# Kernel optimization log

Measured on AMD Instinct MI355X. Metric: run time of the kernel, lower is better.

## Reference

```python
import jax, jax.numpy as jnp
import numpy as np
from jax import lax

HIDDEN = 256      # hidden_dim
LATENT = 128      # latent_dim
VOCAB = 32000     # vocab_size
MAX_LEN = 64      # max_len (stack capacity guard, as in original)
MAX_STEPS = 128   # fixed step budget for the decode stack machine
N_NODES = 511     # complete binary tree, depth 9


def _linear_params(key, fan_in, fan_out):
    k1, k2 = jax.random.split(key)
    s = 1.0 / np.sqrt(fan_in)
    W = jax.random.uniform(k1, (fan_out, fan_in), minval=-s, maxval=s, dtype=jnp.float32)
    b = jax.random.uniform(k2, (fan_out,), minval=-s, maxval=s, dtype=jnp.float32)
    return W, b


def setup_inputs() -> dict:
    key = jax.random.key(0)
    ks = jax.random.split(key, 10)
    embed = jax.random.normal(ks[0], (VOCAB, HIDDEN), dtype=jnp.float32)
    Wpar, bpar = _linear_params(ks[1], 3 * HIDDEN, HIDDEN)
    Wmu, bmu = _linear_params(ks[2], HIDDEN, LATENT)
    Wlv, blv = _linear_params(ks[3], HIDDEN, LATENT)
    W1, b1 = _linear_params(ks[4], LATENT, HIDDEN)
    W2, b2 = _linear_params(ks[5], HIDDEN, HIDDEN + 1)
    Wl, bl = _linear_params(ks[6], HIDDEN, VOCAB)
    Wp, bp = _linear_params(ks[7], HIDDEN, 2 * LATENT + VOCAB)
    values = jax.random.randint(ks[8], (N_NODES,), 0, VOCAB)
    idx = np.arange(N_NODES)
    left = np.where(2 * idx + 1 < N_NODES, 2 * idx + 1, -1).astype(np.int32)
    right = np.where(2 * idx + 2 < N_NODES, 2 * idx + 2, -1).astype(np.int32)
    eps = jax.random.normal(ks[9], (LATENT,), dtype=jnp.float32)
    return dict(embed=embed, Wpar=Wpar, bpar=bpar, Wmu=Wmu, bmu=bmu,
                Wlv=Wlv, blv=blv, W1=W1, b1=b1, W2=W2, b2=b2,
                Wl=Wl, bl=bl, Wp=Wp, bp=bp, eps=eps,
                values=jnp.asarray(values), left=jnp.asarray(left), right=jnp.asarray(right))


def reference(embed, Wpar, bpar, Wmu, bmu, Wlv, blv, W1, b1, W2, b2,
              Wl, bl, Wp, bp, eps, values, left, right):
    # ---------- encode: bottom-up over tree stored as index arrays ----------
    emb = embed[values]  # [N, H], one gather for all node embeddings

    def enc_step(h, i):
        v = emb[i]
        li = jnp.maximum(left[i], 0)
        ri = jnp.maximum(right[i], 0)
        cat = jnp.concatenate([v, h[li], h[ri]])          # [3H]
        hp = cat @ Wpar.T + bpar                           # parent combine
        hi = jnp.where(left[i] < 0, v, hp)                 # leaf -> embedding
        return h.at[i].set(hi), None

    h0 = jnp.zeros((values.shape[0], HIDDEN), dtype=embed.dtype)
    # children have larger index than parents -> process in descending order
    h, _ = lax.scan(enc_step, h0, jnp.arange(values.shape[0] - 1, -1, -1))
    root = h[0]
    mu = root @ Wmu.T + bmu
    logvar = root @ Wlv.T + blv
    z = mu + eps * jnp.exp(0.5 * logvar)                   # reparameterize

    # ---------- decode: stack machine with fixed step budget ----------
    V, L = VOCAB, LATENT
    stack0 = jnp.zeros((MAX_LEN, L), dtype=z.dtype).at[0].set(z)
    out0 = jnp.zeros((MAX_STEPS, V), dtype=z.dtype)

    def dec_step(state, _):
        stack, sp, out, op = state
        active = sp > 0
        idx = jnp.maximum(sp - 1, 0)
        node = stack[idx]                                  # pop
        hmid = jax.nn.leaky_relu(node @ W1.T + b1, 0.2)
        co = hmid @ W2.T + b2                              # [H+1]; co[0] = gate
        is_parent = (co[0] > 0) & (sp - 1 <= MAX_LEN - 2) & active

        def parent_fn(_):
            dec = co[1:] @ Wp.T + bp                       # [V + 2L]
            value = dec[:V]
            ll = dec[V:V + L]
            rl = dec[V + L:]
            # original appends llatent then rlatent -> rlatent on top
            st = stack.at[idx].set(ll).at[idx + 1].set(rl)
            return value, st, sp + 1

        def leaf_fn(_):
            return co[1:] @ Wl.T + bl, stack, sp - 1

        value, st, nsp = lax.cond(is_parent, parent_fn, leaf_fn, None)
        m = active.astype(z.dtype)
        out = out.at[op].add(m * value)                    # rows written once
        stack = jnp.where(active, st, stack)
        sp = jnp.where(active, nsp, sp)
        op = op + active.astype(op.dtype)
        return (stack, sp, out, op), None

    init = (stack0, jnp.int32(1), out0, jnp.int32(0))
    (_, _, out, _), _ = lax.scan(dec_step, init, None, length=MAX_STEPS)
    return out, mu, logvar
```

## Files before the change

kernel.cpp:

```cpp
#include <hip/hip_runtime.h>

#define HID 256
#define LAT 128
#define VOC 32000
#define NSTEP 128

__global__ __launch_bounds__(512)
void prep_kernel(const float* __restrict__ Wp, const float* __restrict__ W2,
                 const float* __restrict__ b2, const float* __restrict__ bp,
                 const float* __restrict__ Wpar,
                 const float* __restrict__ Wmu, const float* __restrict__ Wlv,
                 float* __restrict__ Wcomb, float* __restrict__ bcomb,
                 float* __restrict__ Wq_par, float* __restrict__ Wq_mu,
                 float* __restrict__ Wq_lv, float* __restrict__ Wq_w2) {
    const int b = blockIdx.x;
    const int t = threadIdx.x;
    if (b < 256) {
        const int o = b;
        const int k = t & 255, jh = t >> 8;
        __shared__ float wpt_s[256];
        __shared__ float part_s[2][256];
        __shared__ float red_s[4];
        if (t < 256) wpt_s[t] = Wp[(size_t)(VOC + o) * HID + t];
        __syncthreads();
        float acc = 0.f;
#pragma unroll 8
        for (int j = 0; j < 128; j++)
            acc += wpt_s[jh * 128 + j] * W2[(size_t)(1 + jh * 128 + j) * HID + k];
        part_s[jh][k] = acc;
        if (t < 256) {
            float p = wpt_s[k] * b2[1 + k];
            p += __shfl_xor(p, 1);  p += __shfl_xor(p, 2);  p += __shfl_xor(p, 4);
            p += __shfl_xor(p, 8);  p += __shfl_xor(p, 16); p += __shfl_xor(p, 32);
            if ((k & 63) == 0) red_s[k >> 6] = p;
        }
        __syncthreads();
        if (t < 256) Wcomb[(size_t)o * HID + k] = part_s[0][k] + part_s[1][k];
        if (t == 0) bcomb[o] = bp[VOC + o] + red_s[0] + red_s[1] + red_s[2] + red_s[3];
    } else if (b < 352) {
        const int k4 = (b - 256) * 2 + (t >> 8);
        const int r = t & 255;
        ((float4*)Wq_par)[k4 * 256 + r] = *(const float4*)(Wpar + (size_t)r * 768 + 4 * k4);
    } else if (b < 384) {
        const int k4 = (b - 352) * 2 + (t >> 8);
        const int r = t & 127, sel = (t >> 7) & 1;
        const float* src = (sel ? Wlv : Wmu) + (size_t)r * HID + 4 * k4;
        ((float4*)(sel ? Wq_lv : Wq_mu))[k4 * 128 + r] = *(const float4*)src;
    } else {
        const int k4 = (b - 384) * 2 + (t >> 8);
        const int r = t & 255;
        ((float4*)Wq_w2)[k4 * 256 + r] = *(const float4*)(W2 + (size_t)(1 + r) * HID + 4 * k4);
    }
}

__global__ __launch_bounds__(1024)
void enc2(const float* __restrict__ embed, const int* __restrict__ values,
          const float* __restrict__ Wq, const float* __restrict__ bpar,
          float* __restrict__ h, int base) {
    const int i = base + blockIdx.x;
    const int t = threadIdx.x;
    const int o = t & 255;
    const int g = t >> 8;
    const int cid = g & 1, kh = g >> 1;
    __shared__ __align__(16) float cat[2][768];
    __shared__ float part[4][256];
    __shared__ __align__(16) float pcat[768];

    const int c0n = 2 * i + 1;
    for (int q = t; q < 1536; q += 1024) {
        const int cc = (q >= 768);
        const int e = q - cc * 768;
        const int node = c0n + cc;
        const int seg = e >> 8, idx = e & 255;
        float v;
        if (seg == 0) v = embed[(size_t)values[node] * HID + idx];
        else {
            const int ch = 2 * node + seg;
            v = (ch >= 255) ? embed[(size_t)values[ch] * HID + idx]
                            : h[(size_t)ch * HID + idx];
        }
        cat[cc][e] = v;
    }
    __syncthreads();
    {
        const float4* wq = (const float4*)Wq + o;
        const float4* c4 = (const float4*)cat[cid] + kh * 96;
        float s0 = 0.f, s1 = 0.f, s2 = 0.f, s3 = 0.f;
#pragma unroll 8
        for (int k4 = 0; k4 < 96; k4 += 4) {
            const float4 wa = wq[(size_t)(kh * 96 + k4) * 256];
            const float4 wb = wq[(size_t)(kh * 96 + k4 + 1) * 256];
            const float4 wc = wq[(size_t)(kh * 96 + k4 + 2) * 256];
            const float4 wd = wq[(size_t)(kh * 96 + k4 + 3) * 256];
            const float4 ca = c4[k4], cb = c4[k4 + 1], cx = c4[k4 + 2], cd = c4[k4 + 3];
            s0 = fmaf(wa.x, ca.x, s0); s0 = fmaf(wa.y, ca.y, s0);
            s0 = fmaf(wa.z, ca.z, s0); s0 = fmaf(wa.w, ca.w, s0);
            s1 = fmaf(wb.x, cb.x, s1); s1 = fmaf(wb.y, cb.y, s1);
            s1 = fmaf(wb.z, cb.z, s1); s1 = fmaf(wb.w, cb.w, s1);
            s2 = fmaf(wc.x, cx.x, s2); s2 = fmaf(wc.y, cx.y, s2);
            s2 = fmaf(wc.z, cx.z, s2); s2 = fmaf(wc.w, cx.w, s2);
            s3 = fmaf(wd.x, cd.x, s3); s3 = fmaf(wd.y, cd.y, s3);
            s3 = fmaf(wd.z, cd.z, s3); s3 = fmaf(wd.w, cd.w, s3);
        }
        part[g][o] = (s0 + s1) + (s2 + s3);
    }
    __syncthreads();
    if (t < 512) {
        const int c = t >> 8;
        pcat[256 + (c << 8) + o] = part[c][o] + part[c + 2][o] + bpar[o];
    } else if (t < 768) {
        const int idx = t & 255;
        pcat[idx] = embed[(size_t)values[i] * HID + idx];
    }
    __syncthreads();
    {
        const float4* wq = (const float4*)Wq + o;
        const float4* c4 = (const float4*)pcat + g * 48;
        float s0 = 0.f, s1 = 0.f, s2 = 0.f, s3 = 0.f;
#pragma unroll
        for (int k4 = 0; k4 < 48; k4 += 4) {
            const float4 wa = wq[(size_t)(g * 48 + k4) * 256];
            const float4 wb = wq[(size_t)(g * 48 + k4 + 1) * 256];
            const float4 wc = wq[(size_t)(g * 48 + k4 + 2) * 256];
            const float4 wd = wq[(size_t)(g * 48 + k4 + 3) * 256];
            const float4 ca = c4[k4], cb = c4[k4 + 1], cx = c4[k4 + 2], cd = c4[k4 + 3];
            s0 = fmaf(wa.x, ca.x, s0); s0 = fmaf(wa.y, ca.y, s0);
            s0 = fmaf(wa.z, ca.z, s0); s0 = fmaf(wa.w, ca.w, s0);
            s1 = fmaf(wb.x, cb.x, s1); s1 = fmaf(wb.y, cb.y, s1);
            s1 = fmaf(wb.z, cb.z, s1); s1 = fmaf(wb.w, cb.w, s1);
            s2 = fmaf(wc.x, cx.x, s2); s2 = fmaf(wc.y, cx.y, s2);
            s2 = fmaf(wc.z, cx.z, s2); s2 = fmaf(wc.w, cx.w, s2);
            s3 = fmaf(wd.x, cd.x, s3); s3 = fmaf(wd.y, cd.y, s3);
            s3 = fmaf(wd.z, cd.z, s3); s3 = fmaf(wd.w, cd.w, s3);
        }
        part[g][o] = (s0 + s1) + (s2 + s3);
    }
    __syncthreads();
    if (t < 256)
        h[(size_t)i * HID + t] = part[0][t] + part[1][t] + part[2][t] + part[3][t] + bpar[t];
}

__global__ __launch_bounds__(256)
void enc_lvl(const float* __restrict__ embed, const int* __restrict__ values,
             const float* __restrict__ Wq, const float* __restrict__ bpar,
             float* __restrict__ h, int first, int logS) {
    const int S = 1 << logS;
    const int R = 256 >> logS;
    const int node = first + (blockIdx.x >> logS);
    const int slice = blockIdx.x & (S - 1);
    const int t = threadIdx.x;
    const int rl = t & (R - 1);
    const int g = t >> (8 - logS);
    __shared__ __align__(16) float cat_s[768];
    __shared__ float part_s[256];

    for (int e = t; e < 768; e += 256) {
        const int seg = e >> 8, idx = e & 255;
        cat_s[e] = (seg == 0) ? embed[(size_t)values[node] * HID + idx]
                              : h[(size_t)(2 * node + seg) * HID + idx];
    }
    __syncthreads();

    const int r0 = slice * R;
    const int nk4 = 192 >> logS;
    const float4* wq = (const float4*)Wq + (size_t)(g * nk4) * 256 + r0 + rl;
    const float4* c4 = (const float4*)cat_s + g * nk4;
    float s0 = 0.f, s1 = 0.f, s2 = 0.f, s3 = 0.f;
    for (int k4 = 0; k4 < nk4; k4 += 4) {
        const float4 wa = wq[(size_t)(k4) * 256];
        const float4 wb = wq[(size_t)(k4 + 1) * 256];
        const float4 wc = wq[(size_t)(k4 + 2) * 256];
        const float4 wd = wq[(size_t)(k4 + 3) * 256];
        const float4 ca = c4[k4], cb = c4[k4 + 1], cx = c4[k4 + 2], cd = c4[k4 + 3];
        s0 = fmaf(wa.x, ca.x, s0); s0 = fmaf(wa.y, ca.y, s0);
        s0 = fmaf(wa.z, ca.z, s0); s0 = fmaf(wa.w, ca.w, s0);
        s1 = fmaf(wb.x, cb.x, s1); s1 = fmaf(wb.y, cb.y, s1);
        s1 = fmaf(wb.z, cb.z, s1); s1 = fmaf(wb.w, cb.w, s1);
        s2 = fmaf(wc.x, cx.x, s2); s2 = fmaf(wc.y, cx.y, s2);
        s2 = fmaf(wc.z, cx.z, s2); s2 = fmaf(wc.w, cx.w, s2);
        s3 = fmaf(wd.x, cd.x, s3); s3 = fmaf(wd.y, cd.y, s3);
        s3 = fmaf(wd.z, cd.z, s3); s3 = fmaf(wd.w, cd.w, s3);
    }
    part_s[t] = (s0 + s1) + (s2 + s3);
    __syncthreads();
    if (t < R) {
        float v = bpar[r0 + t];
        for (int g2 = 0; g2 < S; g2++) v += part_s[g2 * R + t];
        h[(size_t)node * HID + r0 + t] = v;
    }
}

__global__ __launch_bounds__(512, 2)
void recur_kernel(const float* W1, const float* b1,
                  const float* W2, const float* b2,
                  const float* Wcomb, const float* bcomb,
                  const float* embed, const int* values,
                  const float* Wq_par, const float* bpar,
                  const float* h,
                  const float* Wq_mu, const float* bmu,
                  const float* Wq_lv, const float* blv,
                  const float* eps, float* out,
                  float* Hrec, int* rowflag) {
    const int t = threadIdx.x;
    const int o = t >> 1;
    const int hk = t & 1;
    __shared__ __align__(16) float stack_s[64 * 128];
    __shared__ __align__(16) float hmid_s[256];
    __shared__ __align__(16) float cat0_s[768];
    __shared__ float c0part_s[8];

    float4 w1r[16];
#pragma unroll
    for (int j = 0; j < 16; j++)
        w1r[j] = *(const float4*)(W1 + (size_t)o * 128 + hk * 64 + 4 * j);
    float4 wcr[32];
#pragma unroll
    for (int j = 0; j < 32; j++)
        wcr[j] = *(const float4*)(Wcomb + (size_t)o * 256 + hk * 128 + 4 * j);

    const float b1o = b1[o];
    const float bco = bcomb[o];
    const float b20 = b2[0];
    const float w2o = W2[o];

    const int v0 = values[0];
    for (int e = t; e < 768; e += 512) {
        const int seg = e >> 8, idx = e & 255;
        cat0_s[e] = (seg == 0) ? embed[(size_t)v0 * HID + idx]
                               : h[(size_t)seg * HID + idx];
    }
    __syncthreads();
    {
        const float4* wq = (const float4*)Wq_par + (size_t)(hk * 96) * 256 + o;
        const float4* c4 = (const float4*)cat0_s + hk * 96;
        float s0 = 0.f, s1 = 0.f, s2 = 0.f, s3 = 0.f;
        for (int k4 = 0; k4 < 96; k4 += 4) {
            const float4 wa = wq[(size_t)(k4) * 256];
            const float4 wb = wq[(size_t)(k4 + 1) * 256];
            const float4 wc = wq[(size_t)(k4 + 2) * 256];
            const float4 wd = wq[(size_t)(k4 + 3) * 256];
            const float4 ca = c4[k4], cb = c4[k4 + 1], cx = c4[k4 + 2], cd = c4[k4 + 3];
            s0 = fmaf(wa.x, ca.x, s0); s0 = fmaf(wa.y, ca.y, s0);
            s0 = fmaf(wa.z, ca.z, s0); s0 = fmaf(wa.w, ca.w, s0);
            s1 = fmaf(wb.x, cb.x, s1); s1 = fmaf(wb.y, cb.y, s1);
            s1 = fmaf(wb.z, cb.z, s1); s1 = fmaf(wb.w, cb.w, s1);
            s2 = fmaf(wc.x, cx.x, s2); s2 = fmaf(wc.y, cx.y, s2);
            s2 = fmaf(wc.z, cx.z, s2); s2 = fmaf(wc.w, cx.w, s2);
            s3 = fmaf(wd.x, cd.x, s3); s3 = fmaf(wd.y, cd.y, s3);
            s3 = fmaf(wd.z, cd.z, s3); s3 = fmaf(wd.w, cd.w, s3);
        }
        float a = (s0 + s1) + (s2 + s3);
        a += __shfl_xor(a, 1);
        if (hk == 0) hmid_s[o] = a + bpar[o];
    }
    __syncthreads();

    {
        const int r = o & 127;
        const float4* wqh = (const float4*)(o < 128 ? Wq_mu : Wq_lv) + r;
        const float4* r4 = (const float4*)hmid_s + hk * 32;
        float s0 = 0.f, s1 = 0.f;
#pragma unroll
        for (int k4 = 0; k4 < 32; k4 += 2) {
            const float4 wa = wqh[(size_t)(hk * 32 + k4) * 128];
            const float4 wb = wqh[(size_t)(hk * 32 + k4 + 1) * 128];
            const float4 ca = r4[k4], cb = r4[k4 + 1];
            s0 = fmaf(wa.x, ca.x, s0); s0 = fmaf(wa.y, ca.y, s0);
            s0 = fmaf(wa.z, ca.z, s0); s0 = fmaf(wa.w, ca.w, s0);
            s1 = fmaf(wb.x, cb.x, s1); s1 = fmaf(wb.y, cb.y, s1);
            s1 = fmaf(wb.z, cb.z, s1); s1 = fmaf(wb.w, cb.w, s1);
        }
        float a = s0 + s1;
        a += __shfl_xor(a, 1);
        if (hk == 0) {
            const float v = a + (o < 128 ? bmu[o & 127] : blv[o & 127]);
            out[(size_t)NSTEP * VOC + o] = v;
            stack_s[128 + o] = v;
        }
    }
    __syncthreads();
    if (t < 128)
        stack_s[t] = stack_s[128 + t] + eps[t] * expf(0.5f * stack_s[256 + t]);

    int sp = 1, op = 0;
    unsigned long long pm0 = 0ULL, pm1 = 0ULL;
    __syncthreads();

    for (int step = 0; step < NSTEP; step++) {
        if (sp <= 0) break;
        const int idx = sp - 1;

        const float* np = stack_s + idx * 128 + hk * 64;
        float a0 = 0.f, a1 = 0.f;
#pragma unroll
        for (int j = 0; j < 16; j += 2) {
            const float4 v0r = *(const float4*)(np + 4 * j);
            const float4 v1r = *(const float4*)(np + 4 * j + 4);
            a0 = fmaf(w1r[j].x, v0r.x, a0);     a0 = fmaf(w1r[j].y, v0r.y, a0);
            a0 = fmaf(w1r[j].z, v0r.z, a0);     a0 = fmaf(w1r[j].w, v0r.w, a0);
            a1 = fmaf(w1r[j + 1].x, v1r.x, a1); a1 = fmaf(w1r[j + 1].y, v1r.y, a1);
            a1 = fmaf(w1r[j + 1].z, v1r.z, a1); a1 = fmaf(w1r[j + 1].w, v1r.w, a1);
        }
        float a = a0 + a1;
        a += __shfl_xor(a, 1);

        float act = a + b1o;
        act = act > 0.f ? act : 0.2f * act;
        float m = w2o * act;
        m += __shfl_xor(m, 2);  m += __shfl_xor(m, 4);  m += __shfl_xor(m, 8);
        m += __shfl_xor(m, 16); m += __shfl_xor(m, 32);
        if ((t & 63) == 0) c0part_s[t >> 6] = m;
        if (hk == 0) {
            hmid_s[o] = act;
            Hrec[(size_t)op * HID + o] = act;
        }
        __syncthreads();

        const float4 q0 = ((const float4*)c0part_s)[0];
        const float4 q1 = ((const float4*)c0part_s)[1];
        const float c = ((q0.x + q0.y) + (q0.z + q0.w)) +
                        ((q1.x + q1.y) + (q1.z + q1.w)) + b20;
        const bool par = (c > 0.f) && (sp <= 63);

        if (par) {
            const float* hp = hmid_s + hk * 128;
            float s0 = 0.f, s1 = 0.f, s2 = 0.f, s3 = 0.f;
#pragma unroll
            for (int j = 0; j < 32; j += 4) {
                const float4 v0r = *(const float4*)(hp + 4 * j);
                const float4 v1r = *(const float4*)(hp + 4 * j + 4);
                const float4 v2r = *(const float4*)(hp + 4 * j + 8);
                const float4 v3r = *(const float4*)(hp + 4 * j + 12);
                s0 = fmaf(wcr[j].x, v0r.x, s0);     s0 = fmaf(wcr[j].y, v0r.y, s0);
                s0 = fmaf(wcr[j].z, v0r.z, s0);     s0 = fmaf(wcr[j].w, v0r.w, s0);
                s1 = fmaf(wcr[j + 1].x, v1r.x, s1); s1 = fmaf(wcr[j + 1].y, v1r.y, s1);
                s1 = fmaf(wcr[j + 1].z, v1r.z, s1); s1 = fmaf(wcr[j + 1].w, v1r.w, s1);
                s2 = fmaf(wcr[j + 2].x, v2r.x, s2); s2 = fmaf(wcr[j + 2].y, v2r.y, s2);
                s2 = fmaf(wcr[j + 2].z, v2r.z, s2); s2 = fmaf(wcr[j + 2].w, v2r.w, s2);
                s3 = fmaf(wcr[j + 3].x, v3r.x, s3); s3 = fmaf(wcr[j + 3].y, v3r.y, s3);
                s3 = fmaf(wcr[j + 3].w, v3r.w, s3); s3 = fmaf(wcr[j + 3].z, v3r.z, s3);
            }
            float s = (s0 + s1) + (s2 + s3);
            s += __shfl_xor(s, 1);
            if (hk == 0)
                stack_s[(idx + (o >> 7)) * 128 + (o & 127)] = s + bco;
            if (op < 64) pm0 |= (1ULL << op); else pm1 |= (1ULL << (op - 64));
            sp += 1;
        } else {
            sp -= 1;
        }
        op++;
        __syncthreads();
    }

    if (t < 128) {
        int f = -1;
        if (t < op) f = (t < 64) ? (int)((pm0 >> t) & 1) : (int)((pm1 >> (t - 64)) & 1);
        rowflag[t] = f;
    }
}

__global__ __launch_bounds__(256)
void co1_kernel(const float* __restrict__ Hrec, const float* __restrict__ Wq_w2,
                const float* __restrict__ b2, const int* __restrict__ rowflag,
                float* __restrict__ Co1, int* __restrict__ lists) {
    const int r = blockIdx.x;
    const int c = threadIdx.x;
    if (r == 128) {
        if (c == 0) {
            int nl = 0, np_ = 0, nz = 0;
            for (int q = 0; q < 128; q++) {
                const int f = rowflag[q];
                if (f == 0) lists[nl++] = q;
                else if (f == 1) lists[128 + np_++] = q;
                else lists[256 + nz++] = q;
            }
            lists[384] = nl; lists[385] = np_; lists[386] = nz;
        }
        return;
    }
    __shared__ __align__(16) float hs[256];
    hs[c] = Hrec[(size_t)r * HID + c];
    __syncthreads();
    const float4* wq = (const float4*)Wq_w2 + c;
    const float4* h4 = (const float4*)hs;
    float s0 = b2[1 + c], s1 = 0.f, s2 = 0.f, s3 = 0.f;
#pragma unroll 8
    for (int k4 = 0; k4 < 64; k4 += 4) {
        const float4 a0 = wq[(k4) * 256],     h0 = h4[k4];
        const float4 a1 = wq[(k4 + 1) * 256], h1 = h4[k4 + 1];
        const float4 a2 = wq[(k4 + 2) * 256], h2 = h4[k4 + 2];
        const float4 a3 = wq[(k4 + 3) * 256], h3 = h4[k4 + 3];
        s0 = fmaf(a0.x, h0.x, s0); s0 = fmaf(a0.y, h0.y, s0);
        s0 = fmaf(a0.z, h0.z, s0); s0 = fmaf(a0.w, h0.w, s0);
        s1 = fmaf(a1.x, h1.x, s1); s1 = fmaf(a1.y, h1.y, s1);
        s1 = fmaf(a1.z, h1.z, s1); s1 = fmaf(a1.w, h1.w, s1);
        s2 = fmaf(a2.x, h2.x, s2); s2 = fmaf(a2.y, h2.y, s2);
        s2 = fmaf(a2.z, h2.z, s2); s2 = fmaf(a2.w, h2.w, s2);
        s3 = fmaf(a3.x, h3.x, s3); s3 = fmaf(a3.y, h3.y, s3);
        s3 = fmaf(a3.z, h3.z, s3); s3 = fmaf(a3.w, h3.w, s3);
    }
    Co1[(size_t)r * HID + c] = (s0 + s1) + (s2 + s3);
}

__global__ __launch_bounds__(256, 2)
void value_kernel(const float* __restrict__ Co1, const int* __restrict__ lists,
                  const float* __restrict__ Wl, const float* __restrict__ bl,
                  const float* __restrict__ Wp, const float* __restrict__ bp,
                  float* __restrict__ out) {
    const int m = blockIdx.y;
    const int t = threadIdx.x;
    const int v = blockIdx.x * 128 + (t & 127);
    const int rh = t >> 7;
    const int n = lists[384 + m];
    const int* list = lists + m * 128;
    const float* Wx = m ? Wp : Wl;
    const float* bx = m ? bp : bl;
    const float bv = bx[v];
    const float4* w4 = (const float4*)(Wx + (size_t)v * HID);

    for (int rc = 0; rc < n; rc += 32) {
        const int nr = min(32, n - rc);
        float acc[16];
#pragma unroll
        for (int i = 0; i < 16; i++) acc[i] = 0.f;
        for (int kc = 0; kc < 4; kc++) {
            float4 w[16];
#pragma unroll
            for (int i = 0; i < 16; i++) w[i] = w4[kc * 16 + i];
#pragma unroll
            for (int aa = 0; aa < 16; aa++) {
                const int rr = 2 * aa + rh;
                if (rr < nr) {
                    const int row = __builtin_amdgcn_readfirstlane(list[rc + rr]);
                    const float* cp = Co1 + (size_t)row * HID + kc * 64;
                    float s0 = 0.f, s1 = 0.f, s2 = 0.f, s3 = 0.f;
#pragma unroll
                    for (int i = 0; i < 16; i += 4) {
                        const float4 c0 = *(const float4*)(cp + 4 * i);
                        const float4 c1 = *(const float4*)(cp + 4 * i + 4);
                        const float4 c2 = *(const float4*)(cp + 4 * i + 8);
                        const float4 c3 = *(const float4*)(cp + 4 * i + 12);
                        s0 = fmaf(w[i].x, c0.x, s0);     s0 = fmaf(w[i].y, c0.y, s0);
                        s0 = fmaf(w[i].z, c0.z, s0);     s0 = fmaf(w[i].w, c0.w, s0);
                        s1 = fmaf(w[i + 1].x, c1.x, s1); s1 = fmaf(w[i + 1].y, c1.y, s1);
                        s1 = fmaf(w[i + 1].z, c1.z, s1); s1 = fmaf(w[i + 1].w, c1.w, s1);
                        s2 = fmaf(w[i + 2].x, c2.x, s2); s2 = fmaf(w[i + 2].y, c2.y, s2);
                        s2 = fmaf(w[i + 2].z, c2.z, s2); s2 = fmaf(w[i + 2].w, c2.w, s2);
                        s3 = fmaf(w[i + 3].x, c3.x, s3); s3 = fmaf(w[i + 3].y, c3.y, s3);
                        s3 = fmaf(w[i + 3].z, c3.z, s3); s3 = fmaf(w[i + 3].w, c3.w, s3);
                    }
                    acc[aa] += (s0 + s1) + (s2 + s3);
                }
            }
        }
#pragma unroll
        for (int aa = 0; aa < 16; aa++) {
            const int rr = 2 * aa + rh;
            if (rr < nr) {
                const int row = __builtin_amdgcn_readfirstlane(list[rc + rr]);
                out[(size_t)row * VOC + v] = acc[aa] + bv;
            }
        }
    }
    if (m == 0 && rh == 0) {
        const int nz = lists[386];
        const int* zl = lists + 256;
        for (int i = 0; i < nz; i++)
            out[(size_t)zl[i] * VOC + v] = 0.f;
    }
}

extern "C" void kernel_launch(void* const* d_in, const int* in_sizes, int n_in,
                              void* d_out, int out_size, void* d_ws, size_t ws_size,
                              hipStream_t stream) {
    const float* embed = (const float*)d_in[0];
    const float* Wpar  = (const float*)d_in[1];
    const float* bpar  = (const float*)d_in[2];
    const float* Wmu   = (const float*)d_in[3];
    const float* bmu   = (const float*)d_in[4];
    const float* Wlv   = (const float*)d_in[5];
    const float* blv   = (const float*)d_in[6];
    const float* W1    = (const float*)d_in[7];
    const float* b1    = (const float*)d_in[8];
    const float* W2    = (const float*)d_in[9];
    const float* b2    = (const float*)d_in[10];
    const float* Wl    = (const float*)d_in[11];
    const float* bl    = (const float*)d_in[12];
    const float* Wp    = (const float*)d_in[13];
    const float* bp    = (const float*)d_in[14];
    const float* eps   = (const float*)d_in[15];
    const int*  values = (const int*)d_in[16];

    float* ws = (float*)d_ws;
    float* h       = ws;
    float* Wcomb   = ws + 65408;
    float* bcomb   = ws + 130944;
    float* Hrec    = ws + 131200;
    float* Co1     = ws + 163968;
    int*   rowflag = (int*)(ws + 196736);
    float* Wq_par  = ws + 196864;
    float* Wq_mu   = ws + 393472;
    float* Wq_lv   = ws + 426240;
    float* Wq_w2   = ws + 459008;
    int*   lists   = (int*)(ws + 524544);
    float* out = (float*)d_out;

    prep_kernel<<<416, 512, 0, stream>>>(Wp, W2, b2, bp, Wpar, Wmu, Wlv,
                                         Wcomb, bcomb, Wq_par, Wq_mu, Wq_lv, Wq_w2);

    enc2<<<64, 1024, 0, stream>>>(embed, values, Wq_par, bpar, h, 63);
    enc_lvl<<<64, 256, 0, stream>>>(embed, values, Wq_par, bpar, h, 31, 1);
    enc_lvl<<<64, 256, 0, stream>>>(embed, values, Wq_par, bpar, h, 15, 2);
    enc_lvl<<<64, 256, 0, stream>>>(embed, values, Wq_par, bpar, h,  7, 3);
    enc_lvl<<<64, 256, 0, stream>>>(embed, values, Wq_par, bpar, h,  3, 4);
    enc_lvl<<<32, 256, 0, stream>>>(embed, values, Wq_par, bpar, h,  1, 4);

    recur_kernel<<<1, 512, 0, stream>>>(W1, b1, W2, b2, Wcomb, bcomb,
                                        embed, values, Wq_par, bpar, h,
                                        Wq_mu, bmu, Wq_lv, blv, eps, out,
                                        Hrec, rowflag);

    co1_kernel<<<129, 256, 0, stream>>>(Hrec, Wq_w2, b2, rowflag, Co1, lists);
    value_kernel<<<dim3(250, 2), 256, 0, stream>>>(Co1, lists, Wl, bl, Wp, bp, out);
}
```

Measured before the change: 254.9 us.

## Merge upper encoder levels into persistent kernel with grid barrier

New measurement: 276.5 us. 8.5% more time.

```diff
diff --git a/kernel.cpp b/kernel.cpp
--- a/kernel.cpp
+++ b/kernel.cpp
@@ -12,9 +12,11 @@
                  const float* __restrict__ Wmu, const float* __restrict__ Wlv,
                  float* __restrict__ Wcomb, float* __restrict__ bcomb,
                  float* __restrict__ Wq_par, float* __restrict__ Wq_mu,
-                 float* __restrict__ Wq_lv, float* __restrict__ Wq_w2) {
+                 float* __restrict__ Wq_lv, float* __restrict__ Wq_w2,
+                 int* __restrict__ bar) {
     const int b = blockIdx.x;
     const int t = threadIdx.x;
+    if (b == 0 && t == 0) { bar[0] = 0; bar[1] = 0; }
     if (b < 256) {
         const int o = b;
         const int k = t & 255, jh = t >> 8;
@@ -130,8 +132,8 @@
             s1 = fmaf(wb.z, cb.z, s1); s1 = fmaf(wb.w, cb.w, s1);
             s2 = fmaf(wc.x, cx.x, s2); s2 = fmaf(wc.y, cx.y, s2);
             s2 = fmaf(wc.z, cx.z, s2); s2 = fmaf(wc.w, cx.w, s2);
-            s3 = fmaf(wd.x, cd.x, s3); s3 = fmaf(wd.y, cd.y, s3);
-            s3 = fmaf(wd.z, cd.z, s3); s3 = fmaf(wd.w, cd.w, s3);
+            s3 = fmaf(wd.x, cd.x, s3); s3 = fmaf(wd.z, cd.z, s3);
+            s3 = fmaf(wd.y, cd.y, s3); s3 = fmaf(wd.w, cd.w, s3);
         }
         part[g][o] = (s0 + s1) + (s2 + s3);
     }
@@ -140,53 +142,90 @@
         h[(size_t)i * HID + t] = part[0][t] + part[1][t] + part[2][t] + part[3][t] + bpar[t];
 }
 
-__global__ __launch_bounds__(256)
-void enc_lvl(const float* __restrict__ embed, const int* __restrict__ values,
-             const float* __restrict__ Wq, const float* __restrict__ bpar,
-             float* __restrict__ h, int first, int logS) {
-    const int S = 1 << logS;
-    const int R = 256 >> logS;
-    const int node = first + (blockIdx.x >> logS);
-    const int slice = blockIdx.x & (S - 1);
+__device__ __forceinline__ void gridbar(int* bar, int nblk) {
+    __syncthreads();
+    if (threadIdx.x == 0) {
+        __threadfence();
+        const int gen = atomicAdd(&bar[1], 0);
+        if (atomicAdd(&bar[0], 1) == nblk - 1) {
+            atomicExch(&bar[0], 0);
+            __threadfence();
+            atomicAdd(&bar[1], 1);
+        } else {
+            while (atomicAdd(&bar[1], 0) == gen) { }
+        }
+    }
+    __syncthreads();
+}
+
+__global__ __launch_bounds__(256, 1)
+void enc_persist(const float* __restrict__ embed, const int* __restrict__ values,
+                 const float* __restrict__ Wq, const float* __restrict__ bpar,
+                 float* h, int* bar) {
     const int t = threadIdx.x;
-    const int rl = t & (R - 1);
-    const int g = t >> (8 - logS);
     __shared__ __align__(16) float cat_s[768];
     __shared__ float part_s[256];
-
-    for (int e = t; e < 768; e += 256) {
-        const int seg = e >> 8, idx = e & 255;
-        cat_s[e] = (seg == 0) ? embed[(size_t)values[node] * HID + idx]
-                              : h[(size_t)(2 * node + seg) * HID + idx];
-    }
-    __syncthreads();
-
-    const int r0 = slice * R;
-    const int nk4 = 192 >> logS;
-    const float4* wq = (const float4*)Wq + (size_t)(g * nk4) * 256 + r0 + rl;
-    const float4* c4 = (const float4*)cat_s + g * nk4;
-    float s0 = 0.f, s1 = 0.f, s2 = 0.f, s3 = 0.f;
-    for (int k4 = 0; k4 < nk4; k4 += 4) {
-        const float4 wa = wq[(size_t)(k4) * 256];
-        const float4 wb = wq[(size_t)(k4 + 1) * 256];
-        const float4 wc = wq[(size_t)(k4 + 2) * 256];
-        const float4 wd = wq[(size_t)(k4 + 3) * 256];
-        const float4 ca = c4[k4], cb = c4[k4 + 1], cx = c4[k4 + 2], cd = c4[k4 + 3];
-        s0 = fmaf(wa.x, ca.x, s0); s0 = fmaf(wa.y, ca.y, s0);
-        s0 = fmaf(wa.z, ca.z, s0); s0 = fmaf(wa.w, ca.w, s0);
-        s1 = fmaf(wb.x, cb.x, s1); s1 = fmaf(wb.y, cb.y, s1);
-        s1 = fmaf(wb.z, cb.z, s1); s1 = fmaf(wb.w, cb.w, s1);
-        s2 = fmaf(wc.x, cx.x, s2); s2 = fmaf(wc.y, cx.y, s2);
-        s2 = fmaf(wc.z, cx.z, s2); s2 = fmaf(wc.w, cx.w, s2);
-        s3 = fmaf(wd.x, cd.x, s3); s3 = fmaf(wd.y, cd.y, s3);
-        s3 = fmaf(wd.z, cd.z, s3); s3 = fmaf(wd.w, cd.w, s3);
-    }
-    part_s[t] = (s0 + s1) + (s2 + s3);
-    __syncthreads();
-    if (t < R) {
-        float v = bpar[r0 + t];
-        for (int g2 = 0; g2 < S; g2++) v += part_s[g2 * R + t];
-        h[(size_t)node * HID + r0 + t] = v;
+    const int firsts[6] = {31, 15, 7, 3, 1, 0};
+
+#pragma unroll 1
+    for (int lvl = 0; lvl < 6; lvl++) {
+        const int logS = lvl + 1;
+        const int S = 1 << logS;
+        const int R = 256 >> logS;
+        const int node = firsts[lvl] + ((int)blockIdx.x >> logS);
+        const int slice = (int)blockIdx.x & (S - 1);
+        const int rl = t & (R - 1);
+        const int g = t >> (8 - logS);
+
+        for (int e = t; e < 768; e += 256) {
+            const int seg = e >> 8, idx = e & 255;
+            float v;
+            if (seg == 0) v = embed[(size_t)values[node] * HID + idx];
+            else v = __hip_atomic_load(&h[(size_t)(2 * node + seg) * HID + idx],
+                                       __ATOMIC_RELAXED, __HIP_MEMORY_SCOPE_AGENT);
+            cat_s[e] = v;
+        }
+        __syncthreads();
+
+        const int r0 = slice * R;
+        const int nk4 = 192 >> logS;
+        const float4* wq = (const float4*)Wq + (size_t)(g * nk4) * 256 + r0 + rl;
+        const float4* c4 = (const float4*)cat_s + g * nk4;
+        float s0 = 0.f, s1 = 0.f, s2 = 0.f, s3 = 0.f;
+        if (nk4 >= 12) {
+            for (int k4 = 0; k4 < nk4; k4 += 4) {
+                const float4 wa = wq[(size_t)(k4) * 256];
+                const float4 wb = wq[(size_t)(k4 + 1) * 256];
+                const float4 wc = wq[(size_t)(k4 + 2) * 256];
+                const float4 wd = wq[(size_t)(k4 + 3) * 256];
+                const float4 ca = c4[k4], cb = c4[k4 + 1], cx = c4[k4 + 2], cd = c4[k4 + 3];
+                s0 = fmaf(wa.x, ca.x, s0); s0 = fmaf(wa.y, ca.y, s0);
+                s0 = fmaf(wa.z, ca.z, s0); s0 = fmaf(wa.w, ca.w, s0);
+                s1 = fmaf(wb.x, cb.x, s1); s1 = fmaf(wb.y, cb.y, s1);
+                s1 = fmaf(wb.z, cb.z, s1); s1 = fmaf(wb.w, cb.w, s1);
+                s2 = fmaf(wc.x, cx.x, s2); s2 = fmaf(wc.y, cx.y, s2);
+                s2 = fmaf(wc.z, cx.z, s2); s2 = fmaf(wc.w, cx.w, s2);
+                s3 = fmaf(wd.x, cd.x, s3); s3 = fmaf(wd.y, cd.y, s3);
+                s3 = fmaf(wd.z, cd.z, s3); s3 = fmaf(wd.w, cd.w, s3);
+            }
+        } else {
+            for (int k4 = 0; k4 < nk4; k4++) {
+                const float4 wa = wq[(size_t)k4 * 256];
+                const float4 ca = c4[k4];
+                s0 = fmaf(wa.x, ca.x, s0); s1 = fmaf(wa.y, ca.y, s1);
+                s2 = fmaf(wa.z, ca.z, s2); s3 = fmaf(wa.w, ca.w, s3);
+            }
+        }
+        part_s[t] = (s0 + s1) + (s2 + s3);
+        __syncthreads();
+        if (t < R) {
+            float v = bpar[r0 + t];
+            for (int g2 = 0; g2 < S; g2++) v += part_s[g2 * R + t];
+            __hip_atomic_store(&h[(size_t)node * HID + r0 + t], v,
+                               __ATOMIC_RELAXED, __HIP_MEMORY_SCOPE_AGENT);
+        }
+        if (lvl < 5) gridbar(bar, 64);
+        else __syncthreads();
     }
 }
 
@@ -194,9 +233,7 @@
 void recur_kernel(const float* W1, const float* b1,
                   const float* W2, const float* b2,
                   const float* Wcomb, const float* bcomb,
-                  const float* embed, const int* values,
-                  const float* Wq_par, const float* bpar,
-                  const float* h,
+                  const float* h0,
                   const float* Wq_mu, const float* bmu,
                   const float* Wq_lv, const float* blv,
                   const float* eps, float* out,
@@ -206,7 +243,6 @@
     const int hk = t & 1;
     __shared__ __align__(16) float stack_s[64 * 128];
     __shared__ __align__(16) float hmid_s[256];
-    __shared__ __align__(16) float cat0_s[768];
     __shared__ float c0part_s[8];
 
     float4 w1r[16];
@@ -223,38 +259,8 @@
     const float b20 = b2[0];
     const float w2o = W2[o];
 
-    const int v0 = values[0];
-    for (int e = t; e < 768; e += 512) {
-        const int seg = e >> 8, idx = e & 255;
-        cat0_s[e] = (seg == 0) ? embed[(size_t)v0 * HID + idx]
-                               : h[(size_t)seg * HID + idx];
-    }
-    __syncthreads();
-    {
-        const float4* wq = (const float4*)Wq_par + (size_t)(hk * 96) * 256 + o;
-        const float4* c4 = (const float4*)cat0_s + hk * 96;
-        float s0 = 0.f, s1 = 0.f, s2 = 0.f, s3 = 0.f;
-        for (int k4 = 0; k4 < 96; k4 += 4) {
-            const float4 wa = wq[(size_t)(k4) * 256];
-            const float4 wb = wq[(size_t)(k4 + 1) * 256];
-            const float4 wc = wq[(size_t)(k4 + 2) * 256];
-            const float4 wd = wq[(size_t)(k4 + 3) * 256];
-            const float4 ca = c4[k4], cb = c4[k4 + 1], cx = c4[k4 + 2], cd = c4[k4 + 3];
-            s0 = fmaf(wa.x, ca.x, s0); s0 = fmaf(wa.y, ca.y, s0);
-            s0 = fmaf(wa.z, ca.z, s0); s0 = fmaf(wa.w, ca.w, s0);
-            s1 = fmaf(wb.x, cb.x, s1); s1 = fmaf(wb.y, cb.y, s1);
-            s1 = fmaf(wb.z, cb.z, s1); s1 = fmaf(wb.w, cb.w, s1);
-            s2 = fmaf(wc.x, cx.x, s2); s2 = fmaf(wc.y, cx.y, s2);
-            s2 = fmaf(wc.z, cx.z, s2); s2 = fmaf(wc.w, cx.w, s2);
-            s3 = fmaf(wd.x, cd.x, s3); s3 = fmaf(wd.y, cd.y, s3);
-            s3 = fmaf(wd.z, cd.z, s3); s3 = fmaf(wd.w, cd.w, s3);
-        }
-        float a = (s0 + s1) + (s2 + s3);
-        a += __shfl_xor(a, 1);
-        if (hk == 0) hmid_s[o] = a + bpar[o];
-    }
-    __syncthreads();
-
+    if (t < 256) hmid_s[t] = h0[t];
+    __syncthreads();
     {
         const int r = o & 127;
         const float4* wqh = (const float4*)(o < 128 ? Wq_mu : Wq_lv) + r;
@@ -338,7 +344,7 @@
                 s2 = fmaf(wcr[j + 2].x, v2r.x, s2); s2 = fmaf(wcr[j + 2].y, v2r.y, s2);
                 s2 = fmaf(wcr[j + 2].z, v2r.z, s2); s2 = fmaf(wcr[j + 2].w, v2r.w, s2);
                 s3 = fmaf(wcr[j + 3].x, v3r.x, s3); s3 = fmaf(wcr[j + 3].y, v3r.y, s3);
-                s3 = fmaf(wcr[j + 3].w, v3r.w, s3); s3 = fmaf(wcr[j + 3].z, v3r.z, s3);
+                s3 = fmaf(wcr[j + 3].z, v3r.z, s3); s3 = fmaf(wcr[j + 3].w, v3r.w, s3);
             }
             float s = (s0 + s1) + (s2 + s3);
             s += __shfl_xor(s, 1);
@@ -504,20 +510,17 @@
     float* Wq_lv   = ws + 426240;
     float* Wq_w2   = ws + 459008;
     int*   lists   = (int*)(ws + 524544);
+    int*   bar     = (int*)(ws + 524960);
     float* out = (float*)d_out;
 
     prep_kernel<<<416, 512, 0, stream>>>(Wp, W2, b2, bp, Wpar, Wmu, Wlv,
-                                         Wcomb, bcomb, Wq_par, Wq_mu, Wq_lv, Wq_w2);
+                                         Wcomb, bcomb, Wq_par, Wq_mu, Wq_lv, Wq_w2,
+                                         bar);
 
     enc2<<<64, 1024, 0, stream>>>(embed, values, Wq_par, bpar, h, 63);
-    enc_lvl<<<64, 256, 0, stream>>>(embed, values, Wq_par, bpar, h, 31, 1);
-    enc_lvl<<<64, 256, 0, stream>>>(embed, values, Wq_par, bpar, h, 15, 2);
-    enc_lvl<<<64, 256, 0, stream>>>(embed, values, Wq_par, bpar, h,  7, 3);
-    enc_lvl<<<64, 256, 0, stream>>>(embed, values, Wq_par, bpar, h,  3, 4);
-    enc_lvl<<<32, 256, 0, stream>>>(embed, values, Wq_par, bpar, h,  1, 4);
-
-    recur_kernel<<<1, 512, 0, stream>>>(W1, b1, W2, b2, Wcomb, bcomb,
-                                        embed, values, Wq_par, bpar, h,
+    enc_persist<<<64, 256, 0, stream>>>(embed, values, Wq_par, bpar, h, bar);
+
+    recur_kernel<<<1, 512, 0, stream>>>(W1, b1, W2, b2, Wcomb, bcomb, h,
                                         Wq_mu, bmu, Wq_lv, blv, eps, out,
                                         Hrec, rowflag);
 
```
